# Kernel tuning notes

Hardware: AMD Instinct MI355X
Metric: run time of the kernel (lower is better)

The kernel has to match this reference:

```python
import jax, jax.numpy as jnp
import numpy as np

SCALE = 256.0
QMIN, QMAX = -32768.0, 32767.0
EPS = 1e-5
NUM_HEADS = 16

def fpq(t):
    return jnp.clip(jnp.round(t * SCALE), QMIN, QMAX) / SCALE

def layer_norm(x, g, b):
    mu = jnp.mean(x, axis=-1, keepdims=True)
    var = jnp.mean(jnp.square(x - mu), axis=-1, keepdims=True)
    return (x - mu) * jax.lax.rsqrt(var + EPS) * g + b

def setup_inputs() -> dict:
    key = jax.random.key(0)
    ks = jax.random.split(key, 10)
    B, S, D, H = 8, 1024, 1024, 4096
    s = 1.0 / np.sqrt(D)
    sh = 1.0 / np.sqrt(H)
    return {
        "x": jax.random.normal(ks[0], (B, S, D), jnp.float32),
        "Wqkv": jax.random.uniform(ks[1], (D, 3 * D), jnp.float32, -s, s),
        "bqkv": jax.random.uniform(ks[2], (3 * D,), jnp.float32, -s, s),
        "Wout": jax.random.uniform(ks[3], (D, D), jnp.float32, -s, s),
        "bout": jax.random.uniform(ks[4], (D,), jnp.float32, -s, s),
        "W1": jax.random.uniform(ks[5], (D, H), jnp.float32, -s, s),
        "b1": jax.random.uniform(ks[6], (H,), jnp.float32, -s, s),
        "W2": jax.random.uniform(ks[7], (H, D), jnp.float32, -sh, sh),
        "b2": jax.random.uniform(ks[8], (D,), jnp.float32, -sh, sh),
        "g1": jnp.ones((D,), jnp.float32),
        "beta1": jnp.zeros((D,), jnp.float32),
        "g2": jnp.ones((D,), jnp.float32),
        "beta2": jnp.zeros((D,), jnp.float32),
    }

def reference(x, Wqkv, bqkv, Wout, bout, W1, b1, W2, b2, g1, beta1, g2, beta2):
    B, S, D = x.shape
    Hh = NUM_HEADS
    hd = D // Hh
    # --- attention on norm1(x) ---
    xn = layer_norm(x, g1, beta1)
    qkv = fpq(xn @ Wqkv + bqkv)                       # [B,S,3D]
    q, k, v = jnp.split(qkv, 3, axis=-1)
    q = q.reshape(B, S, Hh, hd).transpose(0, 2, 1, 3)  # [B,H,S,hd]
    k = k.reshape(B, S, Hh, hd).transpose(0, 2, 1, 3)
    v = v.reshape(B, S, Hh, hd).transpose(0, 2, 1, 3)
    scores = jnp.einsum("bhqd,bhkd->bhqk", q, k) / np.sqrt(hd)
    probs = fpq(jax.nn.softmax(scores, axis=-1))
    ctx = jnp.einsum("bhqk,bhkd->bhqd", probs, v)
    ctx = ctx.transpose(0, 2, 1, 3).reshape(B, S, D)
    attn = fpq(ctx @ Wout + bout)
    x = fpq(x + fpq(attn))
    # --- MLP on norm2(x) ---
    xn2 = layer_norm(x, g2, beta2)
    h = jax.nn.relu(fpq(xn2 @ W1 + b1))
    mlp = fpq(h @ W2 + b2)
    x = fpq(x + fpq(mlp))
    return x
```

## Files before the change

### kernel.cpp

```cpp
#include <hip/hip_runtime.h>
#include <hip/hip_fp16.h>
#include <stdint.h>

typedef _Float16 f16;
typedef _Float16 f16x4 __attribute__((ext_vector_type(4)));
typedef _Float16 f16x8 __attribute__((ext_vector_type(8)));
typedef float f32x4 __attribute__((ext_vector_type(4)));

__device__ __forceinline__ float fpq(float t) {
    float r = rintf(t * 256.0f);
    r = fminf(fmaxf(r, -32768.0f), 32767.0f);
    return r * 0.00390625f;
}

__device__ __forceinline__ int swzkey(int r) { return (r & 3) | ((r >> 1) & 4); }

__device__ __forceinline__ void gll16(const f16* g, f16* l) {
    __builtin_amdgcn_global_load_lds(
        (const __attribute__((address_space(1))) uint32_t*)g,
        (__attribute__((address_space(3))) uint32_t*)l, 16, 0, 0);
}

__global__ __launch_bounds__(256) void ln_kernel(
        const float* __restrict__ x, const float* __restrict__ g,
        const float* __restrict__ b, f16* __restrict__ out) {
    int row = blockIdx.x;
    int t = threadIdx.x;
    const float4* xr = (const float4*)(x + (size_t)row * 1024);
    float4 v = xr[t];
    float s = v.x + v.y + v.z + v.w;
    float s2 = v.x * v.x + v.y * v.y + v.z * v.z + v.w * v.w;
#pragma unroll
    for (int o = 32; o >= 1; o >>= 1) {
        s += __shfl_down(s, o);
        s2 += __shfl_down(s2, o);
    }
    __shared__ float red[8];
    int wid = t >> 6;
    if ((t & 63) == 0) { red[wid] = s; red[4 + wid] = s2; }
    __syncthreads();
    float ts = red[0] + red[1] + red[2] + red[3];
    float ts2 = red[4] + red[5] + red[6] + red[7];
    float mu = ts * (1.0f / 1024.0f);
    float var = ts2 * (1.0f / 1024.0f) - mu * mu;
    float rs = rsqrtf(var + 1e-5f);
    float4 gg = ((const float4*)g)[t];
    float4 bb = ((const float4*)b)[t];
    f16x4 o4;
    o4[0] = (f16)((v.x - mu) * rs * gg.x + bb.x);
    o4[1] = (f16)((v.y - mu) * rs * gg.y + bb.y);
    o4[2] = (f16)((v.z - mu) * rs * gg.z + bb.z);
    o4[3] = (f16)((v.w - mu) * rs * gg.w + bb.w);
    ((f16x4*)out)[(size_t)row * 256 + t] = o4;
}

__global__ __launch_bounds__(256) void transpose_kernel(
        const float* __restrict__ W, f16* __restrict__ WT, int K, int N) {
    __shared__ float tile[32][33];
    int n0 = blockIdx.x * 32, k0 = blockIdx.y * 32;
    int tx = threadIdx.x & 31, ty = threadIdx.x >> 5;
#pragma unroll
    for (int i = 0; i < 32; i += 8)
        tile[ty + i][tx] = W[(size_t)(k0 + ty + i) * N + n0 + tx];
    __syncthreads();
#pragma unroll
    for (int i = 0; i < 32; i += 8)
        WT[(size_t)(n0 + ty + i) * K + k0 + tx] = (f16)tile[tx][ty + i];
}

template <int EPI, int BN>
__global__ __launch_bounds__(512, 2) void gemm8_kernel(
        const f16* __restrict__ A, const f16* __restrict__ BT,
        int N, int K, int GM, int GN,
        const float* __restrict__ bias, const float* __restrict__ resid,
        void* __restrict__ out0, f16* __restrict__ outk, f16* __restrict__ outv) {
    constexpr int WN = (BN == 256) ? 4 : 2;
    constexpr int MF = (BN == 256) ? 8 : 4;
    constexpr int GB = BN / 64;
    constexpr int ABUF = 256 * 64;
    constexpr int BBUF = BN * 64;
    constexpr int BUFSZ = ABUF + BBUF;
    __shared__ f16 lds[2 * BUFSZ];

    int nwg = GM * GN;
    int orig = blockIdx.x;
    int wg = (orig & 7) * (nwg >> 3) + (orig >> 3);
    int bm = wg % GM, bn = wg / GM;
    int m0 = bm * 256, n0 = bn * BN;
    int tid = threadIdx.x;
    int lane = tid & 63;
    int lr = lane & 15, lg = lane >> 4;
    int wv = tid >> 6;
    int wm = wv / WN, wn = wv % WN;

    size_t srcA[4]; int dstA[4];
#pragma unroll
    for (int j = 0; j < 4; ++j) {
        int row = j * 64 + (tid >> 3);
        int slot = (tid & 7) ^ (row & 7);
        srcA[j] = (size_t)(m0 + row) * K + slot * 8;
        dstA[j] = j * 4096 + tid * 8;
    }
    size_t srcB[GB]; int dstB[GB];
#pragma unroll
    for (int j = 0; j < GB; ++j) {
        int row = j * 64 + (tid >> 3);
        int slot = (tid & 7) ^ (row & 7);
        srcB[j] = (size_t)(n0 + row) * K + slot * 8;
        dstB[j] = j * 4096 + tid * 8;
    }

    int offA[2][MF], offB[4][2];
#pragma unroll
    for (int i = 0; i < MF; ++i) {
        int row = wm * (MF * 16) + i * 16 + lr;
#pragma unroll
        for (int kk = 0; kk < 2; ++kk)
            offA[kk][i] = row * 64 + (((kk * 4 + lg) ^ (row & 7)) * 8);
    }
#pragma unroll
    for (int j = 0; j < 4; ++j) {
        int n = wn * 64 + j * 16 + lr;
#pragma unroll
        for (int kk = 0; kk < 2; ++kk)
            offB[j][kk] = ABUF + n * 64 + (((kk * 4 + lg) ^ (n & 7)) * 8);
    }

    f32x4 acc[MF][4] = {};
    int NT = K >> 6;

#pragma unroll
    for (int j = 0; j < 4; ++j) gll16(A + srcA[j], lds + dstA[j]);
#pragma unroll
    for (int j = 0; j < GB; ++j) gll16(BT + srcB[j], lds + ABUF + dstB[j]);
#pragma unroll
    for (int j = 0; j < 4; ++j) gll16(A + srcA[j] + 64, lds + BUFSZ + dstA[j]);
#pragma unroll
    for (int j = 0; j < GB; ++j) gll16(BT + srcB[j] + 64, lds + BUFSZ + ABUF + dstB[j]);
    if constexpr (BN == 256) {
        asm volatile("s_waitcnt vmcnt(8)" ::: "memory");
    } else {
        asm volatile("s_waitcnt vmcnt(6)" ::: "memory");
    }
    __builtin_amdgcn_s_barrier();
    __builtin_amdgcn_sched_barrier(0);

    for (int t = 0; t < NT; ++t) {
        int cur = t & 1;
        f16* Ab = lds + cur * BUFSZ;
        f16x8 a0[MF], a1[MF], b00, b01, b10, b11;
#pragma unroll
        for (int i = 0; i < MF; ++i) a0[i] = *(const f16x8*)&Ab[offA[0][i]];
        b00 = *(const f16x8*)&Ab[offB[0][0]];
        b01 = *(const f16x8*)&Ab[offB[1][0]];
#pragma unroll
        for (int i = 0; i < MF; ++i) a1[i] = *(const f16x8*)&Ab[offA[1][i]];
        b10 = *(const f16x8*)&Ab[offB[0][1]];
        b11 = *(const f16x8*)&Ab[offB[1][1]];
        __builtin_amdgcn_s_setprio(1);
#pragma unroll
        for (int i = 0; i < MF; ++i) {
            acc[i][0] = __builtin_amdgcn_mfma_f32_16x16x32_f16(a0[i], b00, acc[i][0], 0, 0, 0);
            acc[i][1] = __builtin_amdgcn_mfma_f32_16x16x32_f16(a0[i], b01, acc[i][1], 0, 0, 0);
        }
#pragma unroll
        for (int i = 0; i < MF; ++i) {
            acc[i][0] = __builtin_amdgcn_mfma_f32_16x16x32_f16(a1[i], b10, acc[i][0], 0, 0, 0);
            acc[i][1] = __builtin_amdgcn_mfma_f32_16x16x32_f16(a1[i], b11, acc[i][1], 0, 0, 0);
        }
        __builtin_amdgcn_s_setprio(0);
        f16x8 b20 = *(const f16x8*)&Ab[offB[2][0]];
        f16x8 b30 = *(const f16x8*)&Ab[offB[3][0]];
        f16x8 b21 = *(const f16x8*)&Ab[offB[2][1]];
        f16x8 b31 = *(const f16x8*)&Ab[offB[3][1]];
        asm volatile("s_waitcnt lgkmcnt(0)" ::: "memory");
        __builtin_amdgcn_sched_barrier(0);
        __builtin_amdgcn_s_barrier();
        if (t + 2 < NT) {
            size_t kof = (size_t)(t + 2) << 6;
            f16* Bd = Ab + ABUF;
#pragma unroll
            for (int j = 0; j < 4; ++j) gll16(A + srcA[j] + kof, Ab + dstA[j]);
#pragma unroll
            for (int j = 0; j < GB; ++j) gll16(BT + srcB[j] + kof, Bd + dstB[j]);
        }
        __builtin_amdgcn_s_setprio(1);
#pragma unroll
        for (int i = 0; i < MF; ++i) {
            acc[i][2] = __builtin_amdgcn_mfma_f32_16x16x32_f16(a0[i], b20, acc[i][2], 0, 0, 0);
            acc[i][3] = __builtin_amdgcn_mfma_f32_16x16x32_f16(a0[i], b30, acc[i][3], 0, 0, 0);
        }
#pragma unroll
        for (int i = 0; i < MF; ++i) {
            acc[i][2] = __builtin_amdgcn_mfma_f32_16x16x32_f16(a1[i], b21, acc[i][2], 0, 0, 0);
            acc[i][3] = __builtin_amdgcn_mfma_f32_16x16x32_f16(a1[i], b31, acc[i][3], 0, 0, 0);
        }
        __builtin_amdgcn_s_setprio(0);
        if (t + 2 < NT) {
            if constexpr (BN == 256) {
                asm volatile("s_waitcnt vmcnt(8)" ::: "memory");
            } else {
                asm volatile("s_waitcnt vmcnt(6)" ::: "memory");
            }
        } else if (t + 1 < NT) {
            asm volatile("s_waitcnt vmcnt(0)" ::: "memory");
        }
        __builtin_amdgcn_sched_barrier(0);
        __builtin_amdgcn_s_barrier();
    }

#pragma unroll
    for (int i = 0; i < MF; ++i) {
#pragma unroll
        for (int j = 0; j < 4; ++j) {
            int col = n0 + wn * 64 + j * 16 + lr;
            float bv = bias[col];
#pragma unroll
            for (int r = 0; r < 4; ++r) {
                int row = m0 + wm * (MF * 16) + i * 16 + lg * 4 + r;
                float val = acc[i][j][r] + bv;
                if (EPI == 0) {
                    float qv = fpq(val);
                    int part = col >> 10, wi = col & 1023;
                    int hd = wi >> 6, d = wi & 63;
                    int bb = row >> 10, ss = row & 1023;
                    size_t bh = (size_t)(bb * 16 + hd);
                    if (part == 0) {
                        ((f16*)out0)[(bh * 1024 + ss) * 64 + d] = (f16)qv;
                    } else if (part == 1) {
                        outk[bh * 65536 + (ss >> 6) * 4096 + (ss & 63) * 64 + (d ^ (swzkey(ss) << 3))] = (f16)qv;
                    } else {
                        outv[bh * 65536 + (ss >> 6) * 4096 + d * 64 + ((ss & 63) ^ (swzkey(d) << 3))] = (f16)qv;
                    }
                } else if (EPI == 2) {
                    float hv = fmaxf(fpq(val), 0.0f);
                    ((f16*)out0)[(size_t)row * N + col] = (f16)hv;
                } else {
                    float o = fpq(resid[(size_t)row * 1024 + col] + fpq(val));
                    ((float*)out0)[(size_t)row * 1024 + col] = o;
                }
            }
        }
    }
}

__global__ __launch_bounds__(256) void attn_kernel(
        const f16* __restrict__ Q, const f16* __restrict__ Kg,
        const f16* __restrict__ Vt, f16* __restrict__ ctx) {
    int id = blockIdx.x;
    int qt = (id >> 3) & 15;
    int bh = (id >> 7) * 8 + (id & 7);
    int b = bh >> 4, h = bh & 15;
    const f16* Qp = Q + ((size_t)bh * 1024 + (size_t)qt * 64) * 64;
    const f16* Kp = Kg + (size_t)bh * 65536;
    const f16* Vp = Vt + (size_t)bh * 65536;
    int t = threadIdx.x, lane = t & 63, w = t >> 6;
    int lr = lane & 15, lg = lane >> 4;
    __shared__ f16 Ks[4096];
    __shared__ f16 Vs[4096];

    const float L2E = 1.4426950408889634f;
    const float C0 = -24.0f * 1.4426950408889634f;

    f16x8 qf[2];
#pragma unroll
    for (int kk = 0; kk < 2; ++kk) {
        qf[kk] = *(const f16x8*)(Qp + (w * 16 + lr) * 64 + kk * 32 + lg * 8);
#pragma unroll
        for (int j = 0; j < 8; ++j) qf[kk][j] = qf[kk][j] * (f16)0.125f;
    }
    int koff[4][2], voff[4][2];
#pragma unroll
    for (int nf = 0; nf < 4; ++nf) {
        int rowv = 32 * (nf >> 1) + 8 * ((lr >> 2) ^ (2 * (nf & 1))) + 4 * (nf & 1) + (lr & 3);
#pragma unroll
        for (int kk = 0; kk < 2; ++kk)
            koff[nf][kk] = rowv * 64 + (((kk * 4 + lg) ^ swzkey(rowv)) * 8);
    }
#pragma unroll
    for (int db = 0; db < 4; ++db) {
        int d = db * 16 + lr;
#pragma unroll
        for (int kk = 0; kk < 2; ++kk)
            voff[db][kk] = d * 64 + (((kk * 4 + lg) ^ swzkey(d)) * 8);
    }

    float lsum = 0.0f;
    for (int kt = 0; kt < 16; ++kt) {
        __syncthreads();
#pragma unroll
        for (int i = 0; i < 2; ++i) {
            int slot = i * 256 + t;
            gll16(Kp + kt * 4096 + slot * 8, Ks + slot * 8);
        }
        __syncthreads();
        f32x4 sc[4] = {};
#pragma unroll
        for (int kk = 0; kk < 2; ++kk)
#pragma unroll
            for (int nf = 0; nf < 4; ++nf) {
                f16x8 kf = *(const f16x8*)&Ks[koff[nf][kk]];
                sc[nf] = __builtin_amdgcn_mfma_f32_16x16x32_f16(kf, qf[kk], sc[nf], 0, 0, 0);
            }
        float part = 0.0f;
#pragma unroll
        for (int nf = 0; nf < 4; ++nf)
#pragma unroll
            for (int r = 0; r < 4; ++r)
                part += __builtin_amdgcn_exp2f(fmaf(sc[nf][r], L2E, C0));
        lsum += part;
    }
    lsum += __shfl_xor(lsum, 16);
    lsum += __shfl_xor(lsum, 32);
    float rl256 = 256.0f * __builtin_amdgcn_rcpf(lsum);

    f32x4 co[4] = {};
    const float inv256 = 0.00390625f;
    for (int kt = 0; kt < 16; ++kt) {
        __syncthreads();
#pragma unroll
        for (int i = 0; i < 2; ++i) {
            int slot = i * 256 + t;
            gll16(Kp + kt * 4096 + slot * 8, Ks + slot * 8);
            gll16(Vp + kt * 4096 + slot * 8, Vs + slot * 8);
        }
        __syncthreads();
        f32x4 sc[4] = {};
#pragma unroll
        for (int kk = 0; kk < 2; ++kk)
#pragma unroll
            for (int nf = 0; nf < 4; ++nf) {
                f16x8 kf = *(const f16x8*)&Ks[koff[nf][kk]];
                sc[nf] = __builtin_amdgcn_mfma_f32_16x16x32_f16(kf, qf[kk], sc[nf], 0, 0, 0);
            }
        uint32_t pk0[4], pk1[4];
#pragma unroll
        for (int nf = 0; nf < 4; ++nf) {
            float e0 = __builtin_amdgcn_exp2f(fmaf(sc[nf][0], L2E, C0));
            float e1 = __builtin_amdgcn_exp2f(fmaf(sc[nf][1], L2E, C0));
            float e2 = __builtin_amdgcn_exp2f(fmaf(sc[nf][2], L2E, C0));
            float e3 = __builtin_amdgcn_exp2f(fmaf(sc[nf][3], L2E, C0));
            float r0 = rintf(e0 * rl256);
            float r1 = rintf(e1 * rl256);
            float r2 = rintf(e2 * rl256);
            float r3 = rintf(e3 * rl256);
            pk0[nf] = __builtin_bit_cast(uint32_t,
                        __builtin_amdgcn_cvt_pkrtz(r0 * inv256, r1 * inv256));
            pk1[nf] = __builtin_bit_cast(uint32_t,
                        __builtin_amdgcn_cvt_pkrtz(r2 * inv256, r3 * inv256));
        }
#pragma unroll
        for (int kk = 0; kk < 2; ++kk) {
            uint4 fw;
            fw.x = pk0[2 * kk];
            fw.y = pk1[2 * kk];
            fw.z = __shfl_xor(pk0[2 * kk + 1], 32);
            fw.w = __shfl_xor(pk1[2 * kk + 1], 32);
            f16x8 pa = __builtin_bit_cast(f16x8, fw);
#pragma unroll
            for (int db = 0; db < 4; ++db) {
                f16x8 vb = *(const f16x8*)&Vs[voff[db][kk]];
                co[db] = __builtin_amdgcn_mfma_f32_16x16x32_f16(pa, vb, co[db], 0, 0, 0);
            }
        }
    }
#pragma unroll
    for (int db = 0; db < 4; ++db)
#pragma unroll
        for (int r = 0; r < 4; ++r) {
            int ss = qt * 64 + w * 16 + lg * 4 + r;
            ctx[((size_t)b * 1024 + ss) * 1024 + h * 64 + db * 16 + lr] = (f16)co[db][r];
        }
}

extern "C" void kernel_launch(void* const* d_in, const int* in_sizes, int n_in,
                              void* d_out, int out_size, void* d_ws, size_t ws_size,
                              hipStream_t stream) {
    const float* x     = (const float*)d_in[0];
    const float* Wqkv  = (const float*)d_in[1];
    const float* bqkv  = (const float*)d_in[2];
    const float* Wout  = (const float*)d_in[3];
    const float* bout  = (const float*)d_in[4];
    const float* W1    = (const float*)d_in[5];
    const float* b1    = (const float*)d_in[6];
    const float* W2    = (const float*)d_in[7];
    const float* b2    = (const float*)d_in[8];
    const float* g1    = (const float*)d_in[9];
    const float* beta1 = (const float*)d_in[10];
    const float* g2    = (const float*)d_in[11];
    const float* beta2 = (const float*)d_in[12];

    char* ws = (char*)d_ws;
    const size_t MB = 1ull << 20;
    f16*  q_h   = (f16*)(ws);
    f16*  k_h   = (f16*)(ws + 16 * MB);
    f16*  vt_h  = (f16*)(ws + 32 * MB);
    f16*  ctx_h = (f16*)(ws + 48 * MB);
    f16*  h_h   = (f16*)(ws);
    f16*  xn_h  = (f16*)(ws + 64 * MB);
    float* x1   = (float*)(ws + 80 * MB);
    f16*  wT    = (f16*)(ws + 112 * MB);

    ln_kernel<<<8192, 256, 0, stream>>>(x, g1, beta1, xn_h);
    transpose_kernel<<<dim3(96, 32), 256, 0, stream>>>(Wqkv, wT, 1024, 3072);
    gemm8_kernel<0, 256><<<384, 512, 0, stream>>>(xn_h, wT, 3072, 1024, 32, 12, bqkv, nullptr, q_h, k_h, vt_h);
    attn_kernel<<<2048, 256, 0, stream>>>(q_h, k_h, vt_h, ctx_h);
    transpose_kernel<<<dim3(32, 32), 256, 0, stream>>>(Wout, wT, 1024, 1024);
    gemm8_kernel<1, 128><<<256, 512, 0, stream>>>(ctx_h, wT, 1024, 1024, 32, 8, bout, x, x1, nullptr, nullptr);
    ln_kernel<<<8192, 256, 0, stream>>>(x1, g2, beta2, xn_h);
    transpose_kernel<<<dim3(128, 32), 256, 0, stream>>>(W1, wT, 1024, 4096);
    gemm8_kernel<2, 256><<<512, 512, 0, stream>>>(xn_h, wT, 4096, 1024, 32, 16, b1, nullptr, h_h, nullptr, nullptr);
    transpose_kernel<<<dim3(32, 128), 256, 0, stream>>>(W2, wT, 4096, 1024);
    gemm8_kernel<3, 128><<<256, 512, 0, stream>>>(h_h, wT, 1024, 4096, 32, 8, b2, x1, d_out, nullptr, nullptr);
}
```

Baseline: 404.6 us.

## Switch GEMM mainloop to triple-buffered BK=32 stages with split async loads

Halves the K-tile from 64 to 32 and replaces the double-buffered LDS ring with a three-slot ring. The next-next tile's global-to-LDS loads are split between the two MFMA phases, and a new XOR swizzle fits the 32-wide rows. The goal is to keep more loads in flight and hide barrier and memory latency with finer overlap. The cost is twice as many iterations and barriers per K, and less MFMA work between syncs.

```diff
diff --git a/kernel.cpp b/kernel.cpp
--- a/kernel.cpp
+++ b/kernel.cpp
@@ -14,6 +14,7 @@
 }
 
 __device__ __forceinline__ int swzkey(int r) { return (r & 3) | ((r >> 1) & 4); }
+__device__ __forceinline__ int kky(int r) { return (r ^ (r >> 2)) & 3; }
 
 __device__ __forceinline__ void gll16(const f16* g, f16* l) {
     __builtin_amdgcn_global_load_lds(
@@ -76,11 +77,12 @@
         void* __restrict__ out0, f16* __restrict__ outk, f16* __restrict__ outv) {
     constexpr int WN = (BN == 256) ? 4 : 2;
     constexpr int MF = (BN == 256) ? 8 : 4;
-    constexpr int GB = BN / 64;
-    constexpr int ABUF = 256 * 64;
-    constexpr int BBUF = BN * 64;
-    constexpr int BUFSZ = ABUF + BBUF;
-    __shared__ f16 lds[2 * BUFSZ];
+    constexpr int BLN = BN / 128;
+    constexpr int GLOADS = 2 + BLN;
+    constexpr int ABUF = 256 * 32;
+    constexpr int BBUF = BN * 32;
+    constexpr int SLOT = ABUF + BBUF;
+    __shared__ f16 lds[3 * SLOT];
 
     int nwg = GM * GN;
     int orig = blockIdx.x;
@@ -93,120 +95,110 @@
     int wv = tid >> 6;
     int wm = wv / WN, wn = wv % WN;
 
-    size_t srcA[4]; int dstA[4];
-#pragma unroll
-    for (int j = 0; j < 4; ++j) {
-        int row = j * 64 + (tid >> 3);
-        int slot = (tid & 7) ^ (row & 7);
+    size_t srcA[2]; int dstA[2];
+#pragma unroll
+    for (int j = 0; j < 2; ++j) {
+        int row = j * 128 + (tid >> 2);
+        int slot = (tid & 3) ^ kky(row);
         srcA[j] = (size_t)(m0 + row) * K + slot * 8;
         dstA[j] = j * 4096 + tid * 8;
     }
-    size_t srcB[GB]; int dstB[GB];
-#pragma unroll
-    for (int j = 0; j < GB; ++j) {
-        int row = j * 64 + (tid >> 3);
-        int slot = (tid & 7) ^ (row & 7);
+    size_t srcB[BLN]; int dstB[BLN];
+#pragma unroll
+    for (int j = 0; j < BLN; ++j) {
+        int row = j * 128 + (tid >> 2);
+        int slot = (tid & 3) ^ kky(row);
         srcB[j] = (size_t)(n0 + row) * K + slot * 8;
         dstB[j] = j * 4096 + tid * 8;
     }
 
-    int offA[2][MF], offB[4][2];
+    int offA[MF], offB[4];
 #pragma unroll
     for (int i = 0; i < MF; ++i) {
         int row = wm * (MF * 16) + i * 16 + lr;
-#pragma unroll
-        for (int kk = 0; kk < 2; ++kk)
-            offA[kk][i] = row * 64 + (((kk * 4 + lg) ^ (row & 7)) * 8);
+        offA[i] = row * 32 + ((lg ^ kky(row)) * 8);
     }
 #pragma unroll
     for (int j = 0; j < 4; ++j) {
         int n = wn * 64 + j * 16 + lr;
-#pragma unroll
-        for (int kk = 0; kk < 2; ++kk)
-            offB[j][kk] = ABUF + n * 64 + (((kk * 4 + lg) ^ (n & 7)) * 8);
+        offB[j] = ABUF + n * 32 + ((lg ^ kky(n)) * 8);
     }
 
     f32x4 acc[MF][4] = {};
-    int NT = K >> 6;
-
-#pragma unroll
-    for (int j = 0; j < 4; ++j) gll16(A + srcA[j], lds + dstA[j]);
-#pragma unroll
-    for (int j = 0; j < GB; ++j) gll16(BT + srcB[j], lds + ABUF + dstB[j]);
-#pragma unroll
-    for (int j = 0; j < 4; ++j) gll16(A + srcA[j] + 64, lds + BUFSZ + dstA[j]);
-#pragma unroll
-    for (int j = 0; j < GB; ++j) gll16(BT + srcB[j] + 64, lds + BUFSZ + ABUF + dstB[j]);
+    int NT = K >> 5;
+
+#pragma unroll
+    for (int j = 0; j < 2; ++j) gll16(A + srcA[j], lds + dstA[j]);
+#pragma unroll
+    for (int j = 0; j < BLN; ++j) gll16(BT + srcB[j], lds + ABUF + dstB[j]);
+#pragma unroll
+    for (int j = 0; j < 2; ++j) gll16(A + srcA[j] + 32, lds + SLOT + dstA[j]);
+#pragma unroll
+    for (int j = 0; j < BLN; ++j) gll16(BT + srcB[j] + 32, lds + SLOT + ABUF + dstB[j]);
     if constexpr (BN == 256) {
-        asm volatile("s_waitcnt vmcnt(8)" ::: "memory");
+        asm volatile("s_waitcnt vmcnt(4)" ::: "memory");
     } else {
-        asm volatile("s_waitcnt vmcnt(6)" ::: "memory");
+        asm volatile("s_waitcnt vmcnt(3)" ::: "memory");
     }
     __builtin_amdgcn_s_barrier();
     __builtin_amdgcn_sched_barrier(0);
 
+    int cur = 0;
     for (int t = 0; t < NT; ++t) {
-        int cur = t & 1;
-        f16* Ab = lds + cur * BUFSZ;
-        f16x8 a0[MF], a1[MF], b00, b01, b10, b11;
-#pragma unroll
-        for (int i = 0; i < MF; ++i) a0[i] = *(const f16x8*)&Ab[offA[0][i]];
-        b00 = *(const f16x8*)&Ab[offB[0][0]];
-        b01 = *(const f16x8*)&Ab[offB[1][0]];
-#pragma unroll
-        for (int i = 0; i < MF; ++i) a1[i] = *(const f16x8*)&Ab[offA[1][i]];
-        b10 = *(const f16x8*)&Ab[offB[0][1]];
-        b11 = *(const f16x8*)&Ab[offB[1][1]];
-        __builtin_amdgcn_s_setprio(1);
-#pragma unroll
-        for (int i = 0; i < MF; ++i) {
-            acc[i][0] = __builtin_amdgcn_mfma_f32_16x16x32_f16(a0[i], b00, acc[i][0], 0, 0, 0);
-            acc[i][1] = __builtin_amdgcn_mfma_f32_16x16x32_f16(a0[i], b01, acc[i][1], 0, 0, 0);
-        }
-#pragma unroll
-        for (int i = 0; i < MF; ++i) {
-            acc[i][0] = __builtin_amdgcn_mfma_f32_16x16x32_f16(a1[i], b10, acc[i][0], 0, 0, 0);
-            acc[i][1] = __builtin_amdgcn_mfma_f32_16x16x32_f16(a1[i], b11, acc[i][1], 0, 0, 0);
-        }
-        __builtin_amdgcn_s_setprio(0);
-        f16x8 b20 = *(const f16x8*)&Ab[offB[2][0]];
-        f16x8 b30 = *(const f16x8*)&Ab[offB[3][0]];
-        f16x8 b21 = *(const f16x8*)&Ab[offB[2][1]];
-        f16x8 b31 = *(const f16x8*)&Ab[offB[3][1]];
+        f16* S = lds + cur * SLOT;
+        int nx2 = cur + 2; if (nx2 >= 3) nx2 -= 3;
+        f16* S2 = lds + nx2 * SLOT;
+        bool st = (t + 2 < NT);
+        size_t kof = (size_t)(t + 2) << 5;
+        f16x8 a[MF], b0, b1;
+#pragma unroll
+        for (int i = 0; i < MF; ++i) a[i] = *(const f16x8*)&S[offA[i]];
+        b0 = *(const f16x8*)&S[offB[0]];
+        b1 = *(const f16x8*)&S[offB[1]];
+        if (st) {
+            gll16(A + srcA[0] + kof, S2 + dstA[0]);
+            gll16(A + srcA[1] + kof, S2 + dstA[1]);
+        }
+        __builtin_amdgcn_s_barrier();
         asm volatile("s_waitcnt lgkmcnt(0)" ::: "memory");
         __builtin_amdgcn_sched_barrier(0);
+        __builtin_amdgcn_s_setprio(1);
+#pragma unroll
+        for (int i = 0; i < MF; ++i) {
+            acc[i][0] = __builtin_amdgcn_mfma_f32_16x16x32_f16(a[i], b0, acc[i][0], 0, 0, 0);
+            acc[i][1] = __builtin_amdgcn_mfma_f32_16x16x32_f16(a[i], b1, acc[i][1], 0, 0, 0);
+        }
+        __builtin_amdgcn_s_setprio(0);
         __builtin_amdgcn_s_barrier();
-        if (t + 2 < NT) {
-            size_t kof = (size_t)(t + 2) << 6;
-            f16* Bd = Ab + ABUF;
-#pragma unroll
-            for (int j = 0; j < 4; ++j) gll16(A + srcA[j] + kof, Ab + dstA[j]);
-#pragma unroll
-            for (int j = 0; j < GB; ++j) gll16(BT + srcB[j] + kof, Bd + dstB[j]);
-        }
+        f16x8 b2 = *(const f16x8*)&S[offB[2]];
+        f16x8 b3 = *(const f16x8*)&S[offB[3]];
+        if (st) {
+#pragma unroll
+            for (int j = 0; j < BLN; ++j)
+                gll16(BT + srcB[j] + kof, S2 + ABUF + dstB[j]);
+        }
+        __builtin_amdgcn_s_barrier();
+        asm volatile("s_waitcnt lgkmcnt(0)" ::: "memory");
+        __builtin_amdgcn_sched_barrier(0);
         __builtin_amdgcn_s_setprio(1);
 #pragma unroll
         for (int i = 0; i < MF; ++i) {
-            acc[i][2] = __builtin_amdgcn_mfma_f32_16x16x32_f16(a0[i], b20, acc[i][2], 0, 0, 0);
-            acc[i][3] = __builtin_amdgcn_mfma_f32_16x16x32_f16(a0[i], b30, acc[i][3], 0, 0, 0);
-        }
-#pragma unroll
-        for (int i = 0; i < MF; ++i) {
-            acc[i][2] = __builtin_amdgcn_mfma_f32_16x16x32_f16(a1[i], b21, acc[i][2], 0, 0, 0);
-            acc[i][3] = __builtin_amdgcn_mfma_f32_16x16x32_f16(a1[i], b31, acc[i][3], 0, 0, 0);
+            acc[i][2] = __builtin_amdgcn_mfma_f32_16x16x32_f16(a[i], b2, acc[i][2], 0, 0, 0);
+            acc[i][3] = __builtin_amdgcn_mfma_f32_16x16x32_f16(a[i], b3, acc[i][3], 0, 0, 0);
         }
         __builtin_amdgcn_s_setprio(0);
-        if (t + 2 < NT) {
+        if (st) {
             if constexpr (BN == 256) {
-                asm volatile("s_waitcnt vmcnt(8)" ::: "memory");
+                asm volatile("s_waitcnt vmcnt(4)" ::: "memory");
             } else {
-                asm volatile("s_waitcnt vmcnt(6)" ::: "memory");
+                asm volatile("s_waitcnt vmcnt(3)" ::: "memory");
             }
         } else if (t + 1 < NT) {
             asm volatile("s_waitcnt vmcnt(0)" ::: "memory");
         }
         __builtin_amdgcn_sched_barrier(0);
         __builtin_amdgcn_s_barrier();
+        ++cur; if (cur >= 3) cur = 0;
     }
 
 #pragma unroll
```

After: 428.2 us. 1.06x slower.

## Double-buffer GEMM fragment registers and swap tile raster order

Applied to the files above, without the earlier changes.

The GEMM main loop now keeps two register sets of LDS fragments. The next tile's fragments are read from LDS while the MFMAs for the current tile run, so LDS reads overlap compute instead of stalling between the MFMA halves. The loop is unrolled by two with ping-pong register sets, and the global prefetch for t+2 is issued at the start of each step. The block index mapping also changes to iterate N-tiles fastest, which alters L2 reuse. The cost is roughly double the fragment register pressure, which could force spills or lower occupancy under launch_bounds(512,2).

```diff
diff --git a/kernel.cpp b/kernel.cpp
--- a/kernel.cpp
+++ b/kernel.cpp
@@ -19,6 +19,12 @@
     __builtin_amdgcn_global_load_lds(
         (const __attribute__((address_space(1))) uint32_t*)g,
         (__attribute__((address_space(3))) uint32_t*)l, 16, 0, 0);
+}
+
+template <int N> __device__ __forceinline__ void waitvm() {
+    if constexpr (N == 0)      asm volatile("s_waitcnt vmcnt(0)" ::: "memory");
+    else if constexpr (N == 6) asm volatile("s_waitcnt vmcnt(6)" ::: "memory");
+    else                       asm volatile("s_waitcnt vmcnt(8)" ::: "memory");
 }
 
 __global__ __launch_bounds__(256) void ln_kernel(
@@ -77,6 +83,7 @@
     constexpr int WN = (BN == 256) ? 4 : 2;
     constexpr int MF = (BN == 256) ? 8 : 4;
     constexpr int GB = BN / 64;
+    constexpr int GLOADS = 4 + GB;
     constexpr int ABUF = 256 * 64;
     constexpr int BBUF = BN * 64;
     constexpr int BUFSZ = ABUF + BBUF;
@@ -85,7 +92,7 @@
     int nwg = GM * GN;
     int orig = blockIdx.x;
     int wg = (orig & 7) * (nwg >> 3) + (orig >> 3);
-    int bm = wg % GM, bn = wg / GM;
+    int bn = wg % GN, bm = wg / GN;
     int m0 = bm * 256, n0 = bn * BN;
     int tid = threadIdx.x;
     int lane = tid & 63;
@@ -129,85 +136,69 @@
     f32x4 acc[MF][4] = {};
     int NT = K >> 6;
 
-#pragma unroll
-    for (int j = 0; j < 4; ++j) gll16(A + srcA[j], lds + dstA[j]);
-#pragma unroll
-    for (int j = 0; j < GB; ++j) gll16(BT + srcB[j], lds + ABUF + dstB[j]);
-#pragma unroll
-    for (int j = 0; j < 4; ++j) gll16(A + srcA[j] + 64, lds + BUFSZ + dstA[j]);
-#pragma unroll
-    for (int j = 0; j < GB; ++j) gll16(BT + srcB[j] + 64, lds + BUFSZ + ABUF + dstB[j]);
-    if constexpr (BN == 256) {
-        asm volatile("s_waitcnt vmcnt(8)" ::: "memory");
-    } else {
-        asm volatile("s_waitcnt vmcnt(6)" ::: "memory");
-    }
+#define STAGE(DST, TT)                                                          \
+    {   size_t kof_ = (size_t)(TT) << 6;                                        \
+        _Pragma("unroll") for (int j_ = 0; j_ < 4; ++j_)                        \
+            gll16(A + srcA[j_] + kof_, (DST) + dstA[j_]);                       \
+        _Pragma("unroll") for (int j_ = 0; j_ < GB; ++j_)                       \
+            gll16(BT + srcB[j_] + kof_, (DST) + ABUF + dstB[j_]); }
+
+#define READF(SRC, RA0, RA1, RB)                                                \
+    {   _Pragma("unroll") for (int i_ = 0; i_ < MF; ++i_) {                     \
+            RA0[i_] = *(const f16x8*)&(SRC)[offA[0][i_]];                       \
+            RA1[i_] = *(const f16x8*)&(SRC)[offA[1][i_]]; }                     \
+        _Pragma("unroll") for (int j_ = 0; j_ < 4; ++j_) {                      \
+            RB[j_][0] = *(const f16x8*)&(SRC)[offB[j_][0]];                     \
+            RB[j_][1] = *(const f16x8*)&(SRC)[offB[j_][1]]; } }
+
+#define MFMAS(RA0, RA1, RB)                                                     \
+    {   __builtin_amdgcn_s_setprio(1);                                          \
+        _Pragma("unroll") for (int i_ = 0; i_ < MF; ++i_)                       \
+            _Pragma("unroll") for (int j_ = 0; j_ < 4; ++j_)                    \
+                acc[i_][j_] = __builtin_amdgcn_mfma_f32_16x16x32_f16(           \
+                    RA0[i_], RB[j_][0], acc[i_][j_], 0, 0, 0);                  \
+        _Pragma("unroll") for (int i_ = 0; i_ < MF; ++i_)                       \
+            _Pragma("unroll") for (int j_ = 0; j_ < 4; ++j_)                    \
+                acc[i_][j_] = __builtin_amdgcn_mfma_f32_16x16x32_f16(           \
+                    RA1[i_], RB[j_][1], acc[i_][j_], 0, 0, 0);                  \
+        __builtin_amdgcn_s_setprio(0); }
+
+#define STEP(TT, CURB, NXTB, RCA0, RCA1, RCB, RNA0, RNA1, RNB)                  \
+    {   if ((TT) + 2 < NT) STAGE(CURB, (TT) + 2);                               \
+        if ((TT) + 1 < NT) {                                                    \
+            if ((TT) + 2 < NT) { waitvm<GLOADS>(); } else { waitvm<0>(); }      \
+            __builtin_amdgcn_sched_barrier(0);                                  \
+            __builtin_amdgcn_s_barrier();                                       \
+            READF(NXTB, RNA0, RNA1, RNB);                                       \
+        }                                                                       \
+        MFMAS(RCA0, RCA1, RCB);                                                 \
+        if ((TT) + 1 < NT) {                                                    \
+            asm volatile("s_waitcnt lgkmcnt(0)" ::: "memory");                  \
+            __builtin_amdgcn_sched_barrier(0);                                  \
+            __builtin_amdgcn_s_barrier();                                       \
+        }                                                                       \
+    }
+
+    STAGE(lds, 0);
+    STAGE(lds + BUFSZ, 1);
+    waitvm<GLOADS>();
     __builtin_amdgcn_s_barrier();
     __builtin_amdgcn_sched_barrier(0);
-
-    for (int t = 0; t < NT; ++t) {
-        int cur = t & 1;
-        f16* Ab = lds + cur * BUFSZ;
-        f16x8 a0[MF], a1[MF], b00, b01, b10, b11;
-#pragma unroll
-        for (int i = 0; i < MF; ++i) a0[i] = *(const f16x8*)&Ab[offA[0][i]];
-        b00 = *(const f16x8*)&Ab[offB[0][0]];
-        b01 = *(const f16x8*)&Ab[offB[1][0]];
-#pragma unroll
-        for (int i = 0; i < MF; ++i) a1[i] = *(const f16x8*)&Ab[offA[1][i]];
-        b10 = *(const f16x8*)&Ab[offB[0][1]];
-        b11 = *(const f16x8*)&Ab[offB[1][1]];
-        __builtin_amdgcn_s_setprio(1);
-#pragma unroll
-        for (int i = 0; i < MF; ++i) {
-            acc[i][0] = __builtin_amdgcn_mfma_f32_16x16x32_f16(a0[i], b00, acc[i][0], 0, 0, 0);
-            acc[i][1] = __builtin_amdgcn_mfma_f32_16x16x32_f16(a0[i], b01, acc[i][1], 0, 0, 0);
-        }
-#pragma unroll
-        for (int i = 0; i < MF; ++i) {
-            acc[i][0] = __builtin_amdgcn_mfma_f32_16x16x32_f16(a1[i], b10, acc[i][0], 0, 0, 0);
-            acc[i][1] = __builtin_amdgcn_mfma_f32_16x16x32_f16(a1[i], b11, acc[i][1], 0, 0, 0);
-        }
-        __builtin_amdgcn_s_setprio(0);
-        f16x8 b20 = *(const f16x8*)&Ab[offB[2][0]];
-        f16x8 b30 = *(const f16x8*)&Ab[offB[3][0]];
-        f16x8 b21 = *(const f16x8*)&Ab[offB[2][1]];
-        f16x8 b31 = *(const f16x8*)&Ab[offB[3][1]];
-        asm volatile("s_waitcnt lgkmcnt(0)" ::: "memory");
-        __builtin_amdgcn_sched_barrier(0);
-        __builtin_amdgcn_s_barrier();
-        if (t + 2 < NT) {
-            size_t kof = (size_t)(t + 2) << 6;
-            f16* Bd = Ab + ABUF;
-#pragma unroll
-            for (int j = 0; j < 4; ++j) gll16(A + srcA[j] + kof, Ab + dstA[j]);
-#pragma unroll
-            for (int j = 0; j < GB; ++j) gll16(BT + srcB[j] + kof, Bd + dstB[j]);
-        }
-        __builtin_amdgcn_s_setprio(1);
-#pragma unroll
-        for (int i = 0; i < MF; ++i) {
-            acc[i][2] = __builtin_amdgcn_mfma_f32_16x16x32_f16(a0[i], b20, acc[i][2], 0, 0, 0);
-            acc[i][3] = __builtin_amdgcn_mfma_f32_16x16x32_f16(a0[i], b30, acc[i][3], 0, 0, 0);
-        }
-#pragma unroll
-        for (int i = 0; i < MF; ++i) {
-            acc[i][2] = __builtin_amdgcn_mfma_f32_16x16x32_f16(a1[i], b21, acc[i][2], 0, 0, 0);
-            acc[i][3] = __builtin_amdgcn_mfma_f32_16x16x32_f16(a1[i], b31, acc[i][3], 0, 0, 0);
-        }
-        __builtin_amdgcn_s_setprio(0);
-        if (t + 2 < NT) {
-            if constexpr (BN == 256) {
-                asm volatile("s_waitcnt vmcnt(8)" ::: "memory");
-            } else {
-                asm volatile("s_waitcnt vmcnt(6)" ::: "memory");
-            }
-        } else if (t + 1 < NT) {
-            asm volatile("s_waitcnt vmcnt(0)" ::: "memory");
-        }
-        __builtin_amdgcn_sched_barrier(0);
-        __builtin_amdgcn_s_barrier();
-    }
+    f16x8 pa0[MF], pa1[MF], pb[4][2];
+    READF(lds, pa0, pa1, pb);
+    asm volatile("s_waitcnt lgkmcnt(0)" ::: "memory");
+    __builtin_amdgcn_sched_barrier(0);
+    __builtin_amdgcn_s_barrier();
+
+    f16x8 qa0[MF], qa1[MF], qb[4][2];
+    for (int t = 0; t < NT; t += 2) {
+        STEP(t,     lds,         lds + BUFSZ, pa0, pa1, pb, qa0, qa1, qb);
+        STEP(t + 1, lds + BUFSZ, lds,         qa0, qa1, qb, pa0, pa1, pb);
+    }
+#undef STAGE
+#undef READF
+#undef MFMAS
+#undef STEP
 
 #pragma unroll
     for (int i = 0; i < MF; ++i) {
```

Result: slower. 1.183 ms (+192.4%).

## Double-buffer K/V tiles in attention and reorder GEMM workgroup mapping

Applied to the files above, without the earlier changes.

The attention kernel now keeps two LDS buffers for K and V and issues the async global-to-LDS loads for the next tile before computing on the current one. Explicit vmcnt waits and barriers replace the two __syncthreads per iteration, so load latency overlaps with MFMA work. Separately, the GEMM now maps workgroup index with N varying fastest instead of M, which changes which tiles share A/B data in cache. This doubles attention LDS use and leans on hand-counted vmcnt values that must match the number of outstanding loads.

```diff
diff --git a/kernel.cpp b/kernel.cpp
--- a/kernel.cpp
+++ b/kernel.cpp
@@ -19,6 +19,14 @@
     __builtin_amdgcn_global_load_lds(
         (const __attribute__((address_space(1))) uint32_t*)g,
         (__attribute__((address_space(3))) uint32_t*)l, 16, 0, 0);
+}
+
+template <int N> __device__ __forceinline__ void waitvm() {
+    if constexpr (N == 0)      asm volatile("s_waitcnt vmcnt(0)" ::: "memory");
+    else if constexpr (N == 2) asm volatile("s_waitcnt vmcnt(2)" ::: "memory");
+    else if constexpr (N == 4) asm volatile("s_waitcnt vmcnt(4)" ::: "memory");
+    else if constexpr (N == 6) asm volatile("s_waitcnt vmcnt(6)" ::: "memory");
+    else                       asm volatile("s_waitcnt vmcnt(8)" ::: "memory");
 }
 
 __global__ __launch_bounds__(256) void ln_kernel(
@@ -85,7 +93,7 @@
     int nwg = GM * GN;
     int orig = blockIdx.x;
     int wg = (orig & 7) * (nwg >> 3) + (orig >> 3);
-    int bm = wg % GM, bn = wg / GM;
+    int bn = wg % GN, bm = wg / GN;
     int m0 = bm * 256, n0 = bn * BN;
     int tid = threadIdx.x;
     int lane = tid & 63;
@@ -137,11 +145,7 @@
     for (int j = 0; j < 4; ++j) gll16(A + srcA[j] + 64, lds + BUFSZ + dstA[j]);
 #pragma unroll
     for (int j = 0; j < GB; ++j) gll16(BT + srcB[j] + 64, lds + BUFSZ + ABUF + dstB[j]);
-    if constexpr (BN == 256) {
-        asm volatile("s_waitcnt vmcnt(8)" ::: "memory");
-    } else {
-        asm volatile("s_waitcnt vmcnt(6)" ::: "memory");
-    }
+    if constexpr (BN == 256) { waitvm<8>(); } else { waitvm<6>(); }
     __builtin_amdgcn_s_barrier();
     __builtin_amdgcn_sched_barrier(0);
 
@@ -197,13 +201,9 @@
         }
         __builtin_amdgcn_s_setprio(0);
         if (t + 2 < NT) {
-            if constexpr (BN == 256) {
-                asm volatile("s_waitcnt vmcnt(8)" ::: "memory");
-            } else {
-                asm volatile("s_waitcnt vmcnt(6)" ::: "memory");
-            }
+            if constexpr (BN == 256) { waitvm<8>(); } else { waitvm<6>(); }
         } else if (t + 1 < NT) {
-            asm volatile("s_waitcnt vmcnt(0)" ::: "memory");
+            waitvm<0>();
         }
         __builtin_amdgcn_sched_barrier(0);
         __builtin_amdgcn_s_barrier();
@@ -256,8 +256,9 @@
     const f16* Vp = Vt + (size_t)bh * 65536;
     int t = threadIdx.x, lane = t & 63, w = t >> 6;
     int lr = lane & 15, lg = lane >> 4;
-    __shared__ f16 Ks[4096];
-    __shared__ f16 Vs[4096];
+    __shared__ f16 Ks[2][4096];
+    __shared__ f16 Vs[2][4096];
+    int so = t * 8;
 
     const float L2E = 1.4426950408889634f;
     const float C0 = -24.0f * 1.4426950408889634f;
@@ -285,21 +286,27 @@
             voff[db][kk] = d * 64 + (((kk * 4 + lg) ^ swzkey(d)) * 8);
     }
 
+    gll16(Kp + so, Ks[0] + so);
+    gll16(Kp + 2048 + so, Ks[0] + 2048 + so);
     float lsum = 0.0f;
     for (int kt = 0; kt < 16; ++kt) {
-        __syncthreads();
-#pragma unroll
-        for (int i = 0; i < 2; ++i) {
-            int slot = i * 256 + t;
-            gll16(Kp + kt * 4096 + slot * 8, Ks + slot * 8);
-        }
-        __syncthreads();
+        int cur = kt & 1;
+        if (kt < 15) {
+            const f16* src = Kp + (kt + 1) * 4096;
+            gll16(src + so, Ks[cur ^ 1] + so);
+            gll16(src + 2048 + so, Ks[cur ^ 1] + 2048 + so);
+            waitvm<2>();
+        } else {
+            waitvm<0>();
+        }
+        __builtin_amdgcn_sched_barrier(0);
+        __builtin_amdgcn_s_barrier();
         f32x4 sc[4] = {};
 #pragma unroll
         for (int kk = 0; kk < 2; ++kk)
 #pragma unroll
             for (int nf = 0; nf < 4; ++nf) {
-                f16x8 kf = *(const f16x8*)&Ks[koff[nf][kk]];
+                f16x8 kf = *(const f16x8*)&Ks[cur][koff[nf][kk]];
                 sc[nf] = __builtin_amdgcn_mfma_f32_16x16x32_f16(kf, qf[kk], sc[nf], 0, 0, 0);
             }
         float part = 0.0f;
@@ -309,6 +316,7 @@
             for (int r = 0; r < 4; ++r)
                 part += __builtin_amdgcn_exp2f(fmaf(sc[nf][r], L2E, C0));
         lsum += part;
+        __builtin_amdgcn_s_barrier();
     }
     lsum += __shfl_xor(lsum, 16);
     lsum += __shfl_xor(lsum, 32);
@@ -316,21 +324,31 @@
 
     f32x4 co[4] = {};
     const float inv256 = 0.00390625f;
+    gll16(Kp + so, Ks[0] + so);
+    gll16(Kp + 2048 + so, Ks[0] + 2048 + so);
+    gll16(Vp + so, Vs[0] + so);
+    gll16(Vp + 2048 + so, Vs[0] + 2048 + so);
     for (int kt = 0; kt < 16; ++kt) {
-        __syncthreads();
-#pragma unroll
-        for (int i = 0; i < 2; ++i) {
-            int slot = i * 256 + t;
-            gll16(Kp + kt * 4096 + slot * 8, Ks + slot * 8);
-            gll16(Vp + kt * 4096 + slot * 8, Vs + slot * 8);
-        }
-        __syncthreads();
+        int cur = kt & 1;
+        if (kt < 15) {
+            const f16* srck = Kp + (kt + 1) * 4096;
+            const f16* srcv = Vp + (kt + 1) * 4096;
+            gll16(srck + so, Ks[cur ^ 1] + so);
+            gll16(srck + 2048 + so, Ks[cur ^ 1] + 2048 + so);
+            gll16(srcv + so, Vs[cur ^ 1] + so);
+            gll16(srcv + 2048 + so, Vs[cur ^ 1] + 2048 + so);
+            waitvm<4>();
+        } else {
+            waitvm<0>();
+        }
+        __builtin_amdgcn_sched_barrier(0);
+        __builtin_amdgcn_s_barrier();
         f32x4 sc[4] = {};
 #pragma unroll
         for (int kk = 0; kk < 2; ++kk)
 #pragma unroll
             for (int nf = 0; nf < 4; ++nf) {
-                f16x8 kf = *(const f16x8*)&Ks[koff[nf][kk]];
+                f16x8 kf = *(const f16x8*)&Ks[cur][koff[nf][kk]];
                 sc[nf] = __builtin_amdgcn_mfma_f32_16x16x32_f16(kf, qf[kk], sc[nf], 0, 0, 0);
             }
         uint32_t pk0[4], pk1[4];
@@ -359,10 +377,11 @@
             f16x8 pa = __builtin_bit_cast(f16x8, fw);
 #pragma unroll
             for (int db = 0; db < 4; ++db) {
-                f16x8 vb = *(const f16x8*)&Vs[voff[db][kk]];
+                f16x8 vb = *(const f16x8*)&Vs[cur][voff[db][kk]];
                 co[db] = __builtin_amdgcn_mfma_f32_16x16x32_f16(pa, vb, co[db], 0, 0, 0);
             }
         }
+        __builtin_amdgcn_s_barrier();
     }
 #pragma unroll
     for (int db = 0; db < 4; ++db)
```

Measured after the change: 386.5 us. 4.5% less time.
